# Kernel optimization log

Hardware: AMD Instinct MI355X
Metric: run time of the kernel (lower is better)

## Reference

```python
import jax, jax.numpy as jnp
import numpy as np

N, E, G = 50000, 200000, 2000        # nodes, directed edges, graphs in batch
F_IN, HID, HEADS = 64, 128, 4
DM = HID * HEADS                      # 512, concat GAT output dim
EPS = 1e-5
NEG_SLOPE = 0.2                       # PyG GATConv LeakyReLU slope


def setup_inputs() -> dict:
    key = jax.random.key(0)
    ks = jax.random.split(key, 40)
    rn = lambda k, s, sc: jax.random.normal(k, s, jnp.float32) * sc
    inp = {}
    inp["x"] = rn(ks[0], (N, F_IN), 1.0)
    inp["edge_index"] = jax.random.randint(ks[1], (2, E), 0, N)
    inp["batch"] = jnp.sort(jax.random.randint(ks[2], (N,), 0, G))
    dims = [F_IN, DM, DM]
    for l in range(3):
        d = dims[l]
        inp["W%d" % l] = rn(ks[3 + 4 * l], (d, DM), 1.0 / np.sqrt(d))
        inp["as%d" % l] = rn(ks[4 + 4 * l], (HEADS, HID), 0.1)
        inp["ad%d" % l] = rn(ks[5 + 4 * l], (HEADS, HID), 0.1)
        inp["b%d" % l] = jnp.zeros((DM,), jnp.float32)
        inp["g%d" % l] = jnp.ones((DM,), jnp.float32)
        inp["be%d" % l] = jnp.zeros((DM,), jnp.float32)
    inp["c1w"] = rn(ks[20], (2 * DM, HID), 1.0 / np.sqrt(2 * DM))
    inp["c1b"] = jnp.zeros((HID,), jnp.float32)
    inp["c2w"] = rn(ks[21], (HID, HID // 2), 1.0 / np.sqrt(HID))
    inp["c2b"] = jnp.zeros((HID // 2,), jnp.float32)
    inp["c3w"] = rn(ks[22], (HID // 2, 1), 1.0 / np.sqrt(HID // 2))
    inp["c3b"] = jnp.zeros((1,), jnp.float32)
    return inp


def _gat(x, src, dst, W, a_s, a_d, b):
    """PyG GATConv (heads=HEADS, concat) with self-loops already in src/dst."""
    n = x.shape[0]
    h = (x @ W).reshape(n, HEADS, HID)                     # [N,H,D]
    s_src = jnp.sum(h * a_s, -1)                           # [N,H]
    s_dst = jnp.sum(h * a_d, -1)                           # [N,H]
    e = jax.nn.leaky_relu(s_src[src] + s_dst[dst], NEG_SLOPE)  # [Et,H]
    # segment softmax over incoming edges of each dst node (stable)
    m = jax.lax.stop_gradient(jax.ops.segment_max(e, dst, num_segments=n))
    ex = jnp.exp(e - m[dst])
    alpha = ex / jax.ops.segment_sum(ex, dst, num_segments=n)[dst]
    out = jax.ops.segment_sum(h[src] * alpha[:, :, None], dst, num_segments=n)
    return out.reshape(n, HEADS * HID) + b


def _bn(x, g, b):
    mu = jnp.mean(x, 0)
    var = jnp.var(x, 0)
    return (x - mu) * jax.lax.rsqrt(var + EPS) * g + b


def _forward(x, edge_index, batch, layers, c1w, c1b, c2w, c2b, c3w, c3b):
    loops = jnp.arange(N)
    src = jnp.concatenate([edge_index[0], loops])          # add self-loops
    dst = jnp.concatenate([edge_index[1], loops])
    for (W, a_s, a_d, b, g, be) in layers:
        x = jax.nn.relu(_bn(_gat(x, src, dst, W, a_s, a_d, b), g, be))
    cnt = jax.ops.segment_sum(jnp.ones((N,), x.dtype), batch, num_segments=G)
    mean = jax.ops.segment_sum(x, batch, num_segments=G) / jnp.maximum(cnt, 1.0)[:, None]
    mx = jax.ops.segment_max(x, batch, num_segments=G)
    mx = jnp.where(cnt[:, None] > 0, mx, 0.0)
    h = jnp.concatenate([mean, mx], 1)                     # [G, 2*DM]
    h = jax.nn.relu(h @ c1w + c1b)
    h = jax.nn.relu(h @ c2w + c2b)
    return jax.nn.sigmoid(h @ c3w + c3b).squeeze(-1)       # [G]


def reference(x, edge_index, batch, W0, as0, ad0, b0, g0, be0, W1, as1, ad1, b1, g1, be1, W2, as2, ad2, b2, g2, be2, c1w, c1b, c2w, c2b, c3w, c3b):
    layers = [(W0, as0, ad0, b0, g0, be0), (W1, as1, ad1, b1, g1, be1), (W2, as2, ad2, b2, g2, be2)]
    return _forward(x, edge_index, batch, layers, c1w, c1b, c2w, c2b, c3w, c3b)
```

## Files before the change

### kernel.cpp

```cpp
#include <hip/hip_runtime.h>

#define N_NODES 50000
#define E_EDGES 200000
#define ET_EDGES (E_EDGES + N_NODES)
#define G_GRAPHS 2000
#define F_IN 64
#define HID 128
#define HEADS 4
#define DM 512
#define BN_EPS 1e-5f
#define NEG_SLOPE 0.2f
#define YBLK 391
#define NCHUNK (YBLK / 8)

typedef unsigned short ushort_t;
typedef float floatx4 __attribute__((ext_vector_type(4)));
typedef short short8 __attribute__((ext_vector_type(8)));

__device__ __forceinline__ float b2f(unsigned int u) {
    union { unsigned int i; float f; } v; v.i = u << 16; return v.f;
}
__device__ __forceinline__ ushort_t f2b(float f) {
    union { float f; unsigned int i; } v; v.f = f;
    unsigned int r = v.i + 0x7FFFu + ((v.i >> 16) & 1u);
    return (ushort_t)(r >> 16);
}
__device__ __forceinline__ void unpack8(uint4 v, float* f) {
    f[0] = b2f(v.x & 0xffffu); f[1] = b2f(v.x >> 16);
    f[2] = b2f(v.y & 0xffffu); f[3] = b2f(v.y >> 16);
    f[4] = b2f(v.z & 0xffffu); f[5] = b2f(v.z >> 16);
    f[6] = b2f(v.w & 0xffffu); f[7] = b2f(v.w >> 16);
}
__device__ __forceinline__ void glds16(const ushort_t* g, ushort_t* l) {
    __builtin_amdgcn_global_load_lds(
        (const __attribute__((address_space(1))) unsigned int*)g,
        (__attribute__((address_space(3))) unsigned int*)l, 16, 0, 0);
}

#define XN (N_NODES * F_IN)
#define W0N (F_IN * DM)
#define W1N (DM * DM)
__global__ __launch_bounds__(256) void k_prep(const float* __restrict__ x,
                                              const float* __restrict__ w0,
                                              const float* __restrict__ w1,
                                              const float* __restrict__ w2,
                                              ushort_t* __restrict__ Xb,
                                              ushort_t* __restrict__ Wh0,
                                              ushort_t* __restrict__ Wh1,
                                              ushort_t* __restrict__ Wh2) {
    int t = blockIdx.x * 256 + threadIdx.x;
    if (t < XN) { Xb[t] = f2b(x[t]); return; }
    t -= XN;
    if (t < W0N) {
        int k = t >> 9, n = t & 511;
        Wh0[(size_t)n * F_IN + k] = f2b(w0[t]);
        return;
    }
    t -= W0N;
    if (t < W1N) {
        int k = t >> 9, n = t & 511;
        Wh1[(size_t)n * DM + k] = f2b(w1[t]);
        return;
    }
    t -= W1N;
    if (t < W1N) {
        int k = t >> 9, n = t & 511;
        Wh2[(size_t)n * DM + k] = f2b(w2[t]);
    }
}

__global__ __launch_bounds__(256) void k_wsprep(const float* __restrict__ w0,
                                                const float* __restrict__ as0, const float* __restrict__ ad0,
                                                const float* __restrict__ w1,
                                                const float* __restrict__ as1, const float* __restrict__ ad1,
                                                const float* __restrict__ w2,
                                                const float* __restrict__ as2, const float* __restrict__ ad2,
                                                ushort_t* __restrict__ ws0,
                                                ushort_t* __restrict__ ws1,
                                                ushort_t* __restrict__ ws2) {
    int b = blockIdx.x;
    int l = b >> 3, h = (b >> 1) & 3, v = b & 1;
    const float* w = l == 0 ? w0 : l == 1 ? w1 : w2;
    const float* a = v == 0 ? (l == 0 ? as0 : l == 1 ? as1 : as2)
                            : (l == 0 ? ad0 : l == 1 ? ad1 : ad2);
    ushort_t* o = l == 0 ? ws0 : l == 1 ? ws1 : ws2;
    int K = l == 0 ? F_IN : DM;
    __shared__ float av[HID];
    int t = threadIdx.x;
    if (t < HID) av[t] = a[h * HID + t];
    __syncthreads();
    for (int k = t; k < K; k += 256) {
        const float* wr = w + (size_t)k * DM + h * HID;
        float s = 0.f;
#pragma unroll 8
        for (int c = 0; c < HID; ++c) s += wr[c] * av[c];
        o[(h * 2 + v) * K + k] = f2b(s);
    }
}

__global__ __launch_bounds__(256) void k_mgemm(const ushort_t* __restrict__ A,
                                               const ushort_t* __restrict__ Bh,
                                               const ushort_t* __restrict__ ws,
                                               ushort_t* __restrict__ C,
                                               float* __restrict__ ssrc,
                                               float* __restrict__ sdst,
                                               int M, int K) {
    __shared__ __align__(16) ushort_t Ash[3][128 * 32];
    __shared__ __align__(16) ushort_t Bsh[3][128 * 32];
    __shared__ __align__(16) ushort_t wsh[2 * 512];
    int bid = blockIdx.x;
    int head, yb;
    if (bid < NCHUNK * 32) {
        int chunk = bid >> 5, pos = bid & 31;
        yb = chunk * 8 + (pos & 7);
        head = pos >> 3;
    } else {
        int rem = bid - NCHUNK * 32;
        head = rem & 3;
        yb = NCHUNK * 8 + (rem >> 2);
    }
    int m0 = yb * 128, n0 = head * 128;
    int tid = threadIdx.x;
    int lane = tid & 63, wave = tid >> 6;
    int wm = (wave >> 1) * 64, wn = (wave & 1) * 64;
    floatx4 acc[4][4] = {};
    floatx4 sacc[4] = {};
    for (int i = tid; i < 2 * K; i += 256)
        wsh[i] = ws[(size_t)head * 2 * K + i];
    int lrow = lane >> 2, lchunk = lane & 3;
    int fs = (lrow & 3) ^ ((lrow >> 2) & 3);
    int schunk = lchunk ^ fs;
    int ar0 = wave * 16 + lrow;
    int ar1 = ar0 + 64;
    int gr0 = m0 + ar0; if (gr0 >= M) gr0 = M - 1;
    int gr1 = m0 + ar1; if (gr1 >= M) gr1 = M - 1;
    const ushort_t* gA0 = A + (size_t)gr0 * K + schunk * 8;
    const ushort_t* gA1 = A + (size_t)gr1 * K + schunk * 8;
    const ushort_t* gB0 = Bh + (size_t)(n0 + ar0) * K + schunk * 8;
    const ushort_t* gB1 = Bh + (size_t)(n0 + ar1) * K + schunk * 8;
    int rF = lane & 15, q = lane >> 4;
    int swz = ((q ^ (rF & 3) ^ ((rF >> 2) & 3))) * 8;
    ushort_t* As0 = &Ash[0][0]; ushort_t* As1 = &Ash[1][0]; ushort_t* As2 = &Ash[2][0];
    ushort_t* Bs0 = &Bsh[0][0]; ushort_t* Bs1 = &Bsh[1][0]; ushort_t* Bs2 = &Bsh[2][0];
    auto STAGE = [&](ushort_t* Ab, ushort_t* Bb, int koff) {
        glds16(gA0 + koff, Ab + (wave * 16) * 32);
        glds16(gA1 + koff, Ab + (wave * 16 + 64) * 32);
        glds16(gB0 + koff, Bb + (wave * 16) * 32);
        glds16(gB1 + koff, Bb + (wave * 16 + 64) * 32);
    };
    __syncthreads();
    STAGE(As0, Bs0, 0);
    if (K > 32) STAGE(As1, Bs1, 32);
    for (int k0 = 0; k0 < K; k0 += 32) {
        if (k0 + 32 < K) asm volatile("s_waitcnt vmcnt(4)" ::: "memory");
        else             asm volatile("s_waitcnt vmcnt(0)" ::: "memory");
        __builtin_amdgcn_s_barrier();
        __builtin_amdgcn_sched_barrier(0);
        if (k0 + 64 < K) STAGE(As2, Bs2, k0 + 64);
        short8 sf = *(const short8*)&wsh[(rF & 1) * K + q * 8 + k0];
        short8 af[4], bf[4];
#pragma unroll
        for (int i = 0; i < 4; ++i)
            af[i] = *(const short8*)&As0[(wm + i * 16 + rF) * 32 + swz];
#pragma unroll
        for (int j = 0; j < 4; ++j)
            bf[j] = *(const short8*)&Bs0[(wn + j * 16 + rF) * 32 + swz];
#pragma unroll
        for (int i = 0; i < 4; ++i) {
            sacc[i] = __builtin_amdgcn_mfma_f32_16x16x32_bf16(af[i], sf, sacc[i], 0, 0, 0);
#pragma unroll
            for (int j = 0; j < 4; ++j)
                acc[i][j] = __builtin_amdgcn_mfma_f32_16x16x32_bf16(af[i], bf[j], acc[i][j], 0, 0, 0);
        }
        ushort_t* tA = As0; As0 = As1; As1 = As2; As2 = tA;
        ushort_t* tB = Bs0; Bs0 = Bs1; Bs1 = Bs2; Bs2 = tB;
    }
    int cr = (lane >> 4) * 4, cc = lane & 15;
#pragma unroll
    for (int i = 0; i < 4; ++i) {
#pragma unroll
        for (int r = 0; r < 4; ++r) {
            int gr = m0 + wm + i * 16 + cr + r;
            if (gr < M) {
#pragma unroll
                for (int j = 0; j < 4; ++j)
                    C[(size_t)gr * DM + n0 + wn + j * 16 + cc] = f2b(acc[i][j][r]);
                if (cc == 0) ssrc[gr * 4 + head] = sacc[i][r];
                else if (cc == 1) sdst[gr * 4 + head] = sacc[i][r];
            }
        }
    }
}

__global__ __launch_bounds__(256) void k_bnapply(const ushort_t* __restrict__ X,
                                                 const float* __restrict__ stat,
                                                 const float* __restrict__ gam,
                                                 const float* __restrict__ bet,
                                                 ushort_t* __restrict__ Y) {
    __shared__ float sc[512], sh[512];
    int t = threadIdx.x;
    for (int f = t; f < 512; f += 256) {
        float mu = stat[f] * (1.f / (float)N_NODES);
        float var = fmaxf(stat[512 + f] * (1.f / (float)N_NODES) - mu * mu, 0.f);
        float rs = rsqrtf(var + BN_EPS);
        float s = gam[f] * rs;
        sc[f] = s;
        sh[f] = bet[f] - mu * s;
    }
    __syncthreads();
    int c8 = (t & 63) * 8;
    const float* scp = sc + c8;
    const float* shp = sh + c8;
    for (int n = blockIdx.x * 4 + (t >> 6); n < N_NODES; n += gridDim.x * 4) {
        uint4 v = *(const uint4*)&X[(size_t)n * DM + c8];
        float fv[8]; unpack8(v, fv);
        uint4 ov; unsigned* po = (unsigned*)&ov;
#pragma unroll
        for (int j = 0; j < 4; ++j) {
            unsigned lo = f2b(fmaxf(fv[2 * j] * scp[2 * j] + shp[2 * j], 0.f));
            unsigned hi = f2b(fmaxf(fv[2 * j + 1] * scp[2 * j + 1] + shp[2 * j + 1], 0.f));
            po[j] = lo | (hi << 16);
        }
        *(uint4*)&Y[(size_t)n * DM + c8] = ov;
    }
}

__global__ void k_degree(const int* __restrict__ ei, int* __restrict__ deg) {
    int e = blockIdx.x * blockDim.x + threadIdx.x;
    if (e >= ET_EDGES) return;
    int d = (e < E_EDGES) ? ei[E_EDGES + e] : (e - E_EDGES);
    atomicAdd(&deg[d], 1);
}

__global__ __launch_bounds__(1024) void k_scan3(const int* __restrict__ deg,
                                                int* __restrict__ offs,
                                                int* __restrict__ cursor) {
    __shared__ int wsum[16];
    __shared__ int carry;
    int t = threadIdx.x;
    int lane = t & 63, wv = t >> 6;
    if (t == 0) carry = 0;
    __syncthreads();
    for (int base = 0; base < N_NODES; base += 1024) {
        int i = base + t;
        int v = (i < N_NODES) ? deg[i] : 0;
        int x = v;
#pragma unroll
        for (int off = 1; off < 64; off <<= 1) {
            int y = __shfl_up(x, off);
            if (lane >= off) x += y;
        }
        if (lane == 63) wsum[wv] = x;
        __syncthreads();
        int wpre = 0;
#pragma unroll
        for (int w = 0; w < 16; ++w) wpre += (w < wv) ? wsum[w] : 0;
        int incl = wpre + x;
        if (i < N_NODES) { int o = carry + (incl - v); offs[i] = o; cursor[i] = o; }
        __syncthreads();
        if (t == 1023) carry += incl;
        __syncthreads();
    }
    if (t == 0) offs[N_NODES] = carry;
}

__global__ void k_scatter(const int* __restrict__ ei, int* __restrict__ cursor,
                          int* __restrict__ csr_src) {
    int e = blockIdx.x * blockDim.x + threadIdx.x;
    if (e >= ET_EDGES) return;
    int sv, d;
    if (e < E_EDGES) { sv = ei[e]; d = ei[E_EDGES + e]; } else { sv = d = e - E_EDGES; }
    int pos = atomicAdd(&cursor[d], 1);
    csr_src[pos] = sv;
}

__global__ void k_gbounds(const int* __restrict__ batch, int* __restrict__ gstart) {
    int i = blockIdx.x * blockDim.x + threadIdx.x;
    if (i >= N_NODES) return;
    int b = batch[i];
    int p = (i == 0) ? -1 : batch[i - 1];
    for (int g = p + 1; g <= b; ++g) gstart[g] = i;
    if (i == N_NODES - 1)
        for (int g = b + 1; g <= G_GRAPHS; ++g) gstart[g] = N_NODES;
}

__global__ __launch_bounds__(256) void k_aggregate(const ushort_t* __restrict__ H,
                                                   const float* __restrict__ ssrc,
                                                   const float* __restrict__ sdst,
                                                   const int* __restrict__ offs,
                                                   const int* __restrict__ csr_src,
                                                   const float* __restrict__ bias,
                                                   ushort_t* __restrict__ out) {
    int wave = threadIdx.x >> 6, lane = threadIdx.x & 63;
    int n = blockIdx.x * 4 + wave;
    if (n >= N_NODES) return;
    int beg = offs[n], end = offs[n + 1];
    int hl = lane >> 4, li = lane & 15;
    float sdh = sdst[n * 4 + hl];
    float m = -1e30f, s = 0.f;
    for (int e = beg + li; e < end; e += 16) {
        float sc = ssrc[csr_src[e] * 4 + hl] + sdh;
        sc = sc > 0.f ? sc : NEG_SLOPE * sc;
        if (sc > m) { s = s * __expf(m - sc) + 1.f; m = sc; }
        else s += __expf(sc - m);
    }
#pragma unroll
    for (int mk = 1; mk < 16; mk <<= 1) {
        float om = __shfl_xor(m, mk), os = __shfl_xor(s, mk);
        float mn = fmaxf(m, om);
        s = s * __expf(m - mn) + os * __expf(om - mn);
        m = mn;
    }
    float mh = m, inv = 1.f / s;
    float acc[8] = { 0.f, 0.f, 0.f, 0.f, 0.f, 0.f, 0.f, 0.f };
    int e = beg;
    for (; e + 4 <= end; e += 4) {
        int sv0 = csr_src[e], sv1 = csr_src[e + 1];
        int sv2 = csr_src[e + 2], sv3 = csr_src[e + 3];
        float s0 = ssrc[sv0 * 4 + hl], s1 = ssrc[sv1 * 4 + hl];
        float s2 = ssrc[sv2 * 4 + hl], s3 = ssrc[sv3 * 4 + hl];
        uint4 h0 = *(const uint4*)&H[(size_t)sv0 * DM + lane * 8];
        uint4 h1 = *(const uint4*)&H[(size_t)sv1 * DM + lane * 8];
        uint4 h2 = *(const uint4*)&H[(size_t)sv2 * DM + lane * 8];
        uint4 h3 = *(const uint4*)&H[(size_t)sv3 * DM + lane * 8];
        s0 += sdh; s0 = s0 > 0.f ? s0 : NEG_SLOPE * s0;
        s1 += sdh; s1 = s1 > 0.f ? s1 : NEG_SLOPE * s1;
        s2 += sdh; s2 = s2 > 0.f ? s2 : NEG_SLOPE * s2;
        s3 += sdh; s3 = s3 > 0.f ? s3 : NEG_SLOPE * s3;
        float a0 = __expf(s0 - mh) * inv, a1 = __expf(s1 - mh) * inv;
        float a2 = __expf(s2 - mh) * inv, a3 = __expf(s3 - mh) * inv;
        float f0[8], f1[8], f2[8], f3[8];
        unpack8(h0, f0); unpack8(h1, f1); unpack8(h2, f2); unpack8(h3, f3);
#pragma unroll
        for (int j = 0; j < 8; ++j)
            acc[j] += a0 * f0[j] + a1 * f1[j] + a2 * f2[j] + a3 * f3[j];
    }
    for (; e < end; ++e) {
        int sv = csr_src[e];
        float sc = ssrc[sv * 4 + hl] + sdh;
        sc = sc > 0.f ? sc : NEG_SLOPE * sc;
        float alpha = __expf(sc - mh) * inv;
        uint4 hv = *(const uint4*)&H[(size_t)sv * DM + lane * 8];
        float f[8]; unpack8(hv, f);
#pragma unroll
        for (int j = 0; j < 8; ++j) acc[j] += alpha * f[j];
    }
    const float* bp = bias + lane * 8;
    float4 b0 = *(const float4*)bp;
    float4 b1 = *(const float4*)(bp + 4);
    acc[0] += b0.x; acc[1] += b0.y; acc[2] += b0.z; acc[3] += b0.w;
    acc[4] += b1.x; acc[5] += b1.y; acc[6] += b1.z; acc[7] += b1.w;
    uint4 ov; unsigned* po = (unsigned*)&ov;
#pragma unroll
    for (int j = 0; j < 4; ++j)
        po[j] = (unsigned)f2b(acc[2 * j]) | ((unsigned)f2b(acc[2 * j + 1]) << 16);
    *(uint4*)&out[(size_t)n * DM + lane * 8] = ov;
}

#define BN_ROWS 125
__global__ __launch_bounds__(256) void k_bnstats(const ushort_t* __restrict__ X,
                                                 float* __restrict__ stat) {
    int t = threadIdx.x;
    int c2 = t * 2;
    int beg = blockIdx.x * BN_ROWS;
    int end = beg + BN_ROWS; if (end > N_NODES) end = N_NODES;
    float s0 = 0.f, s1 = 0.f, q0 = 0.f, q1 = 0.f;
    for (int n = beg; n < end; ++n) {
        unsigned v = *(const unsigned*)&X[(size_t)n * DM + c2];
        float x0 = b2f(v & 0xffffu), x1 = b2f(v >> 16);
        s0 += x0; s1 += x1;
        q0 += x0 * x0; q1 += x1 * x1;
    }
    atomicAdd(&stat[c2], s0);
    atomicAdd(&stat[c2 + 1], s1);
    atomicAdd(&stat[512 + c2], q0);
    atomicAdd(&stat[512 + c2 + 1], q1);
}

__global__ __launch_bounds__(64) void k_pool(const ushort_t* __restrict__ X,
                                             const int* __restrict__ gstart,
                                             const float* __restrict__ stat,
                                             const float* __restrict__ gam,
                                             const float* __restrict__ bet,
                                             float* __restrict__ pool) {
    int g = blockIdx.x, t = threadIdx.x;
    int beg = gstart[g], end = gstart[g + 1];
    float sc[8], sh[8];
#pragma unroll
    for (int j = 0; j < 8; ++j) {
        int f = t * 8 + j;
        float mu = stat[f] * (1.f / (float)N_NODES);
        float var = fmaxf(stat[512 + f] * (1.f / (float)N_NODES) - mu * mu, 0.f);
        float rs = rsqrtf(var + BN_EPS);
        sc[j] = gam[f] * rs;
        sh[j] = bet[f] - mu * sc[j];
    }
    float sum[8] = { 0 }, mx[8];
#pragma unroll
    for (int j = 0; j < 8; ++j) mx[j] = -1e30f;
    for (int nn = beg; nn < end; ++nn) {
        uint4 xv = *(const uint4*)&X[(size_t)nn * DM + t * 8];
        float f[8]; unpack8(xv, f);
#pragma unroll
        for (int j = 0; j < 8; ++j) {
            f[j] = fmaxf(f[j] * sc[j] + sh[j], 0.f);
            sum[j] += f[j]; mx[j] = fmaxf(mx[j], f[j]);
        }
    }
    float cnt = (float)(end - beg);
    float inv = cnt > 0.f ? 1.f / cnt : 0.f;
#pragma unroll
    for (int j = 0; j < 8; ++j) {
        pool[(size_t)g * 1024 + t * 8 + j] = sum[j] * inv;
        pool[(size_t)g * 1024 + 512 + t * 8 + j] = cnt > 0.f ? mx[j] : 0.f;
    }
}

__global__ __launch_bounds__(256) void k_mlp(const float* __restrict__ pool,
                                             const float* __restrict__ c1w,
                                             const float* __restrict__ c1b,
                                             const float* __restrict__ c2w,
                                             const float* __restrict__ c2b,
                                             const float* __restrict__ c3w,
                                             const float* __restrict__ c3b,
                                             float* __restrict__ out) {
    __shared__ float row[1024];
    __shared__ float part[128];
    __shared__ float h1[128];
    __shared__ float h2[64];
    int g = blockIdx.x, t = threadIdx.x;
    for (int i = t; i < 1024; i += 256) row[i] = pool[(size_t)g * 1024 + i];
    __syncthreads();
    int half = t >> 7, c = t & 127;
    int k0 = half * 512;
    float a1 = 0.f;
#pragma unroll 8
    for (int k = 0; k < 512; ++k) a1 += row[k0 + k] * c1w[(k0 + k) * 128 + c];
    if (half) part[c] = a1;
    __syncthreads();
    if (!half) h1[c] = fmaxf(a1 + part[c] + c1b[c], 0.f);
    __syncthreads();
    if (t < 64) {
        float a2 = c2b[t];
#pragma unroll 8
        for (int k = 0; k < 128; ++k) a2 += h1[k] * c2w[k * 64 + t];
        h2[t] = fmaxf(a2, 0.f);
    }
    __syncthreads();
    if (t < 64) {
        float p = h2[t] * c3w[t];
#pragma unroll
        for (int off = 32; off > 0; off >>= 1) p += __shfl_down(p, off);
        if (t == 0) {
            float z = p + c3b[0];
            out[g] = 1.f / (1.f + __expf(-z));
        }
    }
}

extern "C" void kernel_launch(void* const* d_in, const int* in_sizes, int n_in,
                              void* d_out, int out_size, void* d_ws, size_t ws_size,
                              hipStream_t stream) {
    const float* x = (const float*)d_in[0];
    const int* ei = (const int*)d_in[1];
    const int* batch = (const int*)d_in[2];
    const float* c1w = (const float*)d_in[21];
    const float* c1b = (const float*)d_in[22];
    const float* c2w = (const float*)d_in[23];
    const float* c2b = (const float*)d_in[24];
    const float* c3w = (const float*)d_in[25];
    const float* c3b = (const float*)d_in[26];

    char* p = (char*)d_ws;
    auto carve = [&](size_t bytes) -> char* {
        char* r = p; p += (bytes + 255) & ~(size_t)255; return r;
    };
    ushort_t* buf0   = (ushort_t*)carve((size_t)N_NODES * DM * 2);
    ushort_t* buf1   = (ushort_t*)carve((size_t)N_NODES * DM * 2);
    ushort_t* Xb     = (ushort_t*)carve((size_t)N_NODES * F_IN * 2);
    ushort_t* Wh0    = (ushort_t*)carve((size_t)F_IN * DM * 2);
    ushort_t* Wh1    = (ushort_t*)carve((size_t)DM * DM * 2);
    ushort_t* Wh2    = (ushort_t*)carve((size_t)DM * DM * 2);
    ushort_t* ws0    = (ushort_t*)carve((size_t)8 * F_IN * 2);
    ushort_t* ws1    = (ushort_t*)carve((size_t)8 * DM * 2);
    ushort_t* ws2    = (ushort_t*)carve((size_t)8 * DM * 2);
    float*    ssrc   = (float*)carve((size_t)N_NODES * 4 * 4);
    float*    sdst   = (float*)carve((size_t)N_NODES * 4 * 4);
    int*      deg    = (int*)carve((size_t)N_NODES * 4);
    int*      offs   = (int*)carve((size_t)(N_NODES + 1) * 4);
    int*      cursor = (int*)carve((size_t)N_NODES * 4);
    int*      csrsrc = (int*)carve((size_t)ET_EDGES * 4);
    float*    bnstat = (float*)carve(3 * 1024 * 4);
    int*      gstart = (int*)carve((size_t)(G_GRAPHS + 1) * 4);
    float*    pool   = (float*)carve((size_t)G_GRAPHS * 1024 * 4);

    hipMemsetAsync(deg, 0, (size_t)N_NODES * 4, stream);
    hipMemsetAsync(bnstat, 0, 3 * 1024 * 4, stream);
    k_degree<<<(ET_EDGES + 255) / 256, 256, 0, stream>>>(ei, deg);
    k_scan3<<<1, 1024, 0, stream>>>(deg, offs, cursor);
    k_scatter<<<(ET_EDGES + 255) / 256, 256, 0, stream>>>(ei, cursor, csrsrc);
    k_gbounds<<<(N_NODES + 255) / 256, 256, 0, stream>>>(batch, gstart);
    {
        int total = XN + W0N + 2 * W1N;
        k_prep<<<(total + 255) / 256, 256, 0, stream>>>(
            x, (const float*)d_in[3], (const float*)d_in[9], (const float*)d_in[15],
            Xb, Wh0, Wh1, Wh2);
    }
    k_wsprep<<<24, 256, 0, stream>>>(
        (const float*)d_in[3], (const float*)d_in[4], (const float*)d_in[5],
        (const float*)d_in[9], (const float*)d_in[10], (const float*)d_in[11],
        (const float*)d_in[15], (const float*)d_in[16], (const float*)d_in[17],
        ws0, ws1, ws2);

    const ushort_t* Whs[3] = { Wh0, Wh1, Wh2 };
    const ushort_t* wss[3] = { ws0, ws1, ws2 };
    const float* pgam = nullptr;
    const float* pbet = nullptr;
    const ushort_t* in = Xb;
    for (int l = 0; l < 3; ++l) {
        int K = (l == 0) ? F_IN : DM;
        const float* bia = (const float*)d_in[6 + 6 * l];
        const float* gam = (const float*)d_in[7 + 6 * l];
        const float* bet = (const float*)d_in[8 + 6 * l];
        ushort_t* h   = (l % 2 == 0) ? buf1 : buf0;
        ushort_t* agg = (l % 2 == 0) ? buf0 : buf1;

        k_mgemm<<<4 * YBLK, 256, 0, stream>>>(
            in, Whs[l], wss[l], h, ssrc, sdst, N_NODES, K);
        k_aggregate<<<(N_NODES + 3) / 4, 256, 0, stream>>>(h, ssrc, sdst, offs, csrsrc, bia, agg);
        k_bnstats<<<(N_NODES + BN_ROWS - 1) / BN_ROWS, 256, 0, stream>>>(agg, bnstat + l * 1024);
        if (l < 2)
            k_bnapply<<<2048, 256, 0, stream>>>(agg, bnstat + l * 1024, gam, bet, h);
        in = h;
        pgam = gam; pbet = bet;
    }
    k_pool<<<G_GRAPHS, 64, 0, stream>>>(buf0, gstart, bnstat + 2 * 1024, pgam, pbet, pool);
    k_mlp<<<G_GRAPHS, 256, 0, stream>>>(pool, c1w, c1b, c2w, c2b, c3w, c3b,
                                        (float*)d_out);
}
```

Baseline: 707.9 us.

## Fuse BN stats into aggregation, parallelize CSR scan, fuse pooling with MLP

Three changes. The single-block serial prefix scan becomes a three-kernel multi-block scan. BatchNorm sum and sum-of-squares are accumulated inside the aggregation kernel, with each wave handling 8 nodes and per-block atomics, so the separate stats pass that re-read the 50000x512 activation is gone. Graph pooling is merged into the MLP kernel so the intermediate pool buffer and one launch disappear. The costs are fewer blocks in aggregation (32 nodes per block) and statistics taken from fp32 accumulators before bf16 rounding, which differs slightly from the old path.

```diff
diff --git a/kernel.cpp b/kernel.cpp
--- a/kernel.cpp
+++ b/kernel.cpp
@@ -12,6 +12,8 @@
 #define NEG_SLOPE 0.2f
 #define YBLK 391
 #define NCHUNK (YBLK / 8)
+#define NBLK 49
+#define AGG_NPB 32
 
 typedef unsigned short ushort_t;
 typedef float floatx4 __attribute__((ext_vector_type(4)));
@@ -232,36 +234,63 @@
     atomicAdd(&deg[d], 1);
 }
 
-__global__ __launch_bounds__(1024) void k_scan3(const int* __restrict__ deg,
+__global__ __launch_bounds__(1024) void k_scanA(const int* __restrict__ deg,
+                                                int* __restrict__ bsum) {
+    __shared__ int wsum[16];
+    int t = threadIdx.x, lane = t & 63, wv = t >> 6;
+    int i = blockIdx.x * 1024 + t;
+    int v = (i < N_NODES) ? deg[i] : 0;
+#pragma unroll
+    for (int off = 32; off > 0; off >>= 1) v += __shfl_down(v, off);
+    if (lane == 0) wsum[wv] = v;
+    __syncthreads();
+    if (t == 0) {
+        int s = 0;
+#pragma unroll
+        for (int w = 0; w < 16; ++w) s += wsum[w];
+        bsum[blockIdx.x] = s;
+    }
+}
+
+__global__ __launch_bounds__(64) void k_scanB(const int* __restrict__ bsum,
+                                              int* __restrict__ bpre,
+                                              int* __restrict__ offs) {
+    int l = threadIdx.x;
+    int v = (l < NBLK) ? bsum[l] : 0;
+    int x = v;
+#pragma unroll
+    for (int off = 1; off < 64; off <<= 1) {
+        int y = __shfl_up(x, off);
+        if (l >= off) x += y;
+    }
+    if (l < NBLK) bpre[l] = x - v;
+    if (l == NBLK - 1) offs[N_NODES] = x;
+}
+
+__global__ __launch_bounds__(1024) void k_scanC(const int* __restrict__ deg,
+                                                const int* __restrict__ bpre,
                                                 int* __restrict__ offs,
                                                 int* __restrict__ cursor) {
     __shared__ int wsum[16];
-    __shared__ int carry;
-    int t = threadIdx.x;
-    int lane = t & 63, wv = t >> 6;
-    if (t == 0) carry = 0;
-    __syncthreads();
-    for (int base = 0; base < N_NODES; base += 1024) {
-        int i = base + t;
-        int v = (i < N_NODES) ? deg[i] : 0;
-        int x = v;
-#pragma unroll
-        for (int off = 1; off < 64; off <<= 1) {
-            int y = __shfl_up(x, off);
-            if (lane >= off) x += y;
-        }
-        if (lane == 63) wsum[wv] = x;
-        __syncthreads();
-        int wpre = 0;
-#pragma unroll
-        for (int w = 0; w < 16; ++w) wpre += (w < wv) ? wsum[w] : 0;
-        int incl = wpre + x;
-        if (i < N_NODES) { int o = carry + (incl - v); offs[i] = o; cursor[i] = o; }
-        __syncthreads();
-        if (t == 1023) carry += incl;
-        __syncthreads();
-    }
-    if (t == 0) offs[N_NODES] = carry;
+    int t = threadIdx.x, lane = t & 63, wv = t >> 6;
+    int i = blockIdx.x * 1024 + t;
+    int v = (i < N_NODES) ? deg[i] : 0;
+    int x = v;
+#pragma unroll
+    for (int off = 1; off < 64; off <<= 1) {
+        int y = __shfl_up(x, off);
+        if (lane >= off) x += y;
+    }
+    if (lane == 63) wsum[wv] = x;
+    __syncthreads();
+    int wpre = 0;
+#pragma unroll
+    for (int w = 0; w < 16; ++w) wpre += (w < wv) ? wsum[w] : 0;
+    int incl = wpre + x;
+    if (i < N_NODES) {
+        int o = bpre[blockIdx.x] + incl - v;
+        offs[i] = o; cursor[i] = o;
+    }
 }
 
 __global__ void k_scatter(const int* __restrict__ ei, int* __restrict__ cursor,
@@ -284,152 +313,142 @@
         for (int g = b + 1; g <= G_GRAPHS; ++g) gstart[g] = N_NODES;
 }
 
-__global__ __launch_bounds__(256) void k_aggregate(const ushort_t* __restrict__ H,
-                                                   const float* __restrict__ ssrc,
-                                                   const float* __restrict__ sdst,
-                                                   const int* __restrict__ offs,
-                                                   const int* __restrict__ csr_src,
-                                                   const float* __restrict__ bias,
-                                                   ushort_t* __restrict__ out) {
-    int wave = threadIdx.x >> 6, lane = threadIdx.x & 63;
-    int n = blockIdx.x * 4 + wave;
-    if (n >= N_NODES) return;
-    int beg = offs[n], end = offs[n + 1];
+__global__ __launch_bounds__(256) void k_aggstats(const ushort_t* __restrict__ H,
+                                                  const float* __restrict__ ssrc,
+                                                  const float* __restrict__ sdst,
+                                                  const int* __restrict__ offs,
+                                                  const int* __restrict__ csr_src,
+                                                  const float* __restrict__ bias,
+                                                  ushort_t* __restrict__ out,
+                                                  float* __restrict__ stat) {
+    __shared__ float sS[4][512], sQ[4][512];
+    int tid = threadIdx.x;
+    int wave = tid >> 6, lane = tid & 63;
     int hl = lane >> 4, li = lane & 15;
-    float sdh = sdst[n * 4 + hl];
-    float m = -1e30f, s = 0.f;
-    for (int e = beg + li; e < end; e += 16) {
-        float sc = ssrc[csr_src[e] * 4 + hl] + sdh;
-        sc = sc > 0.f ? sc : NEG_SLOPE * sc;
-        if (sc > m) { s = s * __expf(m - sc) + 1.f; m = sc; }
-        else s += __expf(sc - m);
-    }
-#pragma unroll
-    for (int mk = 1; mk < 16; mk <<= 1) {
-        float om = __shfl_xor(m, mk), os = __shfl_xor(s, mk);
-        float mn = fmaxf(m, om);
-        s = s * __expf(m - mn) + os * __expf(om - mn);
-        m = mn;
-    }
-    float mh = m, inv = 1.f / s;
-    float acc[8] = { 0.f, 0.f, 0.f, 0.f, 0.f, 0.f, 0.f, 0.f };
-    int e = beg;
-    for (; e + 4 <= end; e += 4) {
-        int sv0 = csr_src[e], sv1 = csr_src[e + 1];
-        int sv2 = csr_src[e + 2], sv3 = csr_src[e + 3];
-        float s0 = ssrc[sv0 * 4 + hl], s1 = ssrc[sv1 * 4 + hl];
-        float s2 = ssrc[sv2 * 4 + hl], s3 = ssrc[sv3 * 4 + hl];
-        uint4 h0 = *(const uint4*)&H[(size_t)sv0 * DM + lane * 8];
-        uint4 h1 = *(const uint4*)&H[(size_t)sv1 * DM + lane * 8];
-        uint4 h2 = *(const uint4*)&H[(size_t)sv2 * DM + lane * 8];
-        uint4 h3 = *(const uint4*)&H[(size_t)sv3 * DM + lane * 8];
-        s0 += sdh; s0 = s0 > 0.f ? s0 : NEG_SLOPE * s0;
-        s1 += sdh; s1 = s1 > 0.f ? s1 : NEG_SLOPE * s1;
-        s2 += sdh; s2 = s2 > 0.f ? s2 : NEG_SLOPE * s2;
-        s3 += sdh; s3 = s3 > 0.f ? s3 : NEG_SLOPE * s3;
-        float a0 = __expf(s0 - mh) * inv, a1 = __expf(s1 - mh) * inv;
-        float a2 = __expf(s2 - mh) * inv, a3 = __expf(s3 - mh) * inv;
-        float f0[8], f1[8], f2[8], f3[8];
-        unpack8(h0, f0); unpack8(h1, f1); unpack8(h2, f2); unpack8(h3, f3);
-#pragma unroll
-        for (int j = 0; j < 8; ++j)
-            acc[j] += a0 * f0[j] + a1 * f1[j] + a2 * f2[j] + a3 * f3[j];
-    }
-    for (; e < end; ++e) {
-        int sv = csr_src[e];
-        float sc = ssrc[sv * 4 + hl] + sdh;
-        sc = sc > 0.f ? sc : NEG_SLOPE * sc;
-        float alpha = __expf(sc - mh) * inv;
-        uint4 hv = *(const uint4*)&H[(size_t)sv * DM + lane * 8];
-        float f[8]; unpack8(hv, f);
-#pragma unroll
-        for (int j = 0; j < 8; ++j) acc[j] += alpha * f[j];
-    }
     const float* bp = bias + lane * 8;
     float4 b0 = *(const float4*)bp;
     float4 b1 = *(const float4*)(bp + 4);
-    acc[0] += b0.x; acc[1] += b0.y; acc[2] += b0.z; acc[3] += b0.w;
-    acc[4] += b1.x; acc[5] += b1.y; acc[6] += b1.z; acc[7] += b1.w;
-    uint4 ov; unsigned* po = (unsigned*)&ov;
-#pragma unroll
-    for (int j = 0; j < 4; ++j)
-        po[j] = (unsigned)f2b(acc[2 * j]) | ((unsigned)f2b(acc[2 * j + 1]) << 16);
-    *(uint4*)&out[(size_t)n * DM + lane * 8] = ov;
-}
-
-#define BN_ROWS 125
-__global__ __launch_bounds__(256) void k_bnstats(const ushort_t* __restrict__ X,
-                                                 float* __restrict__ stat) {
-    int t = threadIdx.x;
-    int c2 = t * 2;
-    int beg = blockIdx.x * BN_ROWS;
-    int end = beg + BN_ROWS; if (end > N_NODES) end = N_NODES;
-    float s0 = 0.f, s1 = 0.f, q0 = 0.f, q1 = 0.f;
-    for (int n = beg; n < end; ++n) {
-        unsigned v = *(const unsigned*)&X[(size_t)n * DM + c2];
-        float x0 = b2f(v & 0xffffu), x1 = b2f(v >> 16);
-        s0 += x0; s1 += x1;
-        q0 += x0 * x0; q1 += x1 * x1;
-    }
-    atomicAdd(&stat[c2], s0);
-    atomicAdd(&stat[c2 + 1], s1);
-    atomicAdd(&stat[512 + c2], q0);
-    atomicAdd(&stat[512 + c2 + 1], q1);
-}
-
-__global__ __launch_bounds__(64) void k_pool(const ushort_t* __restrict__ X,
-                                             const int* __restrict__ gstart,
-                                             const float* __restrict__ stat,
-                                             const float* __restrict__ gam,
-                                             const float* __restrict__ bet,
-                                             float* __restrict__ pool) {
-    int g = blockIdx.x, t = threadIdx.x;
-    int beg = gstart[g], end = gstart[g + 1];
-    float sc[8], sh[8];
+    float sa[8] = { 0.f }, qa[8] = { 0.f };
+    int nbase = blockIdx.x * AGG_NPB + wave * 8;
+    for (int ni = 0; ni < 8; ++ni) {
+        int n = nbase + ni;
+        if (n < N_NODES) {
+            int beg = offs[n], end = offs[n + 1];
+            float sdh = sdst[n * 4 + hl];
+            float m = -1e30f, s = 0.f;
+            for (int e = beg + li; e < end; e += 16) {
+                float sc = ssrc[csr_src[e] * 4 + hl] + sdh;
+                sc = sc > 0.f ? sc : NEG_SLOPE * sc;
+                if (sc > m) { s = s * __expf(m - sc) + 1.f; m = sc; }
+                else s += __expf(sc - m);
+            }
+#pragma unroll
+            for (int mk = 1; mk < 16; mk <<= 1) {
+                float om = __shfl_xor(m, mk), os = __shfl_xor(s, mk);
+                float mn = fmaxf(m, om);
+                s = s * __expf(m - mn) + os * __expf(om - mn);
+                m = mn;
+            }
+            float mh = m, inv = 1.f / s;
+            float acc[8] = { 0.f, 0.f, 0.f, 0.f, 0.f, 0.f, 0.f, 0.f };
+            int e = beg;
+            for (; e + 4 <= end; e += 4) {
+                int sv0 = csr_src[e], sv1 = csr_src[e + 1];
+                int sv2 = csr_src[e + 2], sv3 = csr_src[e + 3];
+                float s0 = ssrc[sv0 * 4 + hl], s1 = ssrc[sv1 * 4 + hl];
+                float s2 = ssrc[sv2 * 4 + hl], s3 = ssrc[sv3 * 4 + hl];
+                uint4 h0 = *(const uint4*)&H[(size_t)sv0 * DM + lane * 8];
+                uint4 h1 = *(const uint4*)&H[(size_t)sv1 * DM + lane * 8];
+                uint4 h2 = *(const uint4*)&H[(size_t)sv2 * DM + lane * 8];
+                uint4 h3 = *(const uint4*)&H[(size_t)sv3 * DM + lane * 8];
+                s0 += sdh; s0 = s0 > 0.f ? s0 : NEG_SLOPE * s0;
+                s1 += sdh; s1 = s1 > 0.f ? s1 : NEG_SLOPE * s1;
+                s2 += sdh; s2 = s2 > 0.f ? s2 : NEG_SLOPE * s2;
+                s3 += sdh; s3 = s3 > 0.f ? s3 : NEG_SLOPE * s3;
+                float a0 = __expf(s0 - mh) * inv, a1 = __expf(s1 - mh) * inv;
+                float a2 = __expf(s2 - mh) * inv, a3 = __expf(s3 - mh) * inv;
+                float f0[8], f1[8], f2[8], f3[8];
+                unpack8(h0, f0); unpack8(h1, f1); unpack8(h2, f2); unpack8(h3, f3);
+#pragma unroll
+                for (int j = 0; j < 8; ++j)
+                    acc[j] += a0 * f0[j] + a1 * f1[j] + a2 * f2[j] + a3 * f3[j];
+            }
+            for (; e < end; ++e) {
+                int sv = csr_src[e];
+                float sc = ssrc[sv * 4 + hl] + sdh;
+                sc = sc > 0.f ? sc : NEG_SLOPE * sc;
+                float alpha = __expf(sc - mh) * inv;
+                uint4 hv = *(const uint4*)&H[(size_t)sv * DM + lane * 8];
+                float f[8]; unpack8(hv, f);
+#pragma unroll
+                for (int j = 0; j < 8; ++j) acc[j] += alpha * f[j];
+            }
+            acc[0] += b0.x; acc[1] += b0.y; acc[2] += b0.z; acc[3] += b0.w;
+            acc[4] += b1.x; acc[5] += b1.y; acc[6] += b1.z; acc[7] += b1.w;
+            uint4 ov; unsigned* po = (unsigned*)&ov;
+#pragma unroll
+            for (int j = 0; j < 4; ++j)
+                po[j] = (unsigned)f2b(acc[2 * j]) | ((unsigned)f2b(acc[2 * j + 1]) << 16);
+            *(uint4*)&out[(size_t)n * DM + lane * 8] = ov;
+#pragma unroll
+            for (int j = 0; j < 8; ++j) {
+                sa[j] += acc[j];
+                qa[j] += acc[j] * acc[j];
+            }
+        }
+    }
 #pragma unroll
     for (int j = 0; j < 8; ++j) {
-        int f = t * 8 + j;
-        float mu = stat[f] * (1.f / (float)N_NODES);
-        float var = fmaxf(stat[512 + f] * (1.f / (float)N_NODES) - mu * mu, 0.f);
-        float rs = rsqrtf(var + BN_EPS);
-        sc[j] = gam[f] * rs;
-        sh[j] = bet[f] - mu * sc[j];
-    }
-    float sum[8] = { 0 }, mx[8];
-#pragma unroll
-    for (int j = 0; j < 8; ++j) mx[j] = -1e30f;
-    for (int nn = beg; nn < end; ++nn) {
-        uint4 xv = *(const uint4*)&X[(size_t)nn * DM + t * 8];
-        float f[8]; unpack8(xv, f);
-#pragma unroll
-        for (int j = 0; j < 8; ++j) {
-            f[j] = fmaxf(f[j] * sc[j] + sh[j], 0.f);
-            sum[j] += f[j]; mx[j] = fmaxf(mx[j], f[j]);
-        }
-    }
-    float cnt = (float)(end - beg);
-    float inv = cnt > 0.f ? 1.f / cnt : 0.f;
-#pragma unroll
-    for (int j = 0; j < 8; ++j) {
-        pool[(size_t)g * 1024 + t * 8 + j] = sum[j] * inv;
-        pool[(size_t)g * 1024 + 512 + t * 8 + j] = cnt > 0.f ? mx[j] : 0.f;
-    }
-}
-
-__global__ __launch_bounds__(256) void k_mlp(const float* __restrict__ pool,
-                                             const float* __restrict__ c1w,
-                                             const float* __restrict__ c1b,
-                                             const float* __restrict__ c2w,
-                                             const float* __restrict__ c2b,
-                                             const float* __restrict__ c3w,
-                                             const float* __restrict__ c3b,
-                                             float* __restrict__ out) {
+        sS[wave][lane * 8 + j] = sa[j];
+        sQ[wave][lane * 8 + j] = qa[j];
+    }
+    __syncthreads();
+    for (int f = tid; f < 512; f += 256) {
+        atomicAdd(&stat[f], sS[0][f] + sS[1][f] + sS[2][f] + sS[3][f]);
+        atomicAdd(&stat[512 + f], sQ[0][f] + sQ[1][f] + sQ[2][f] + sQ[3][f]);
+    }
+}
+
+__global__ __launch_bounds__(256) void k_poolmlp(const ushort_t* __restrict__ X,
+                                                 const int* __restrict__ gstart,
+                                                 const float* __restrict__ stat,
+                                                 const float* __restrict__ gam,
+                                                 const float* __restrict__ bet,
+                                                 const float* __restrict__ c1w,
+                                                 const float* __restrict__ c1b,
+                                                 const float* __restrict__ c2w,
+                                                 const float* __restrict__ c2b,
+                                                 const float* __restrict__ c3w,
+                                                 const float* __restrict__ c3b,
+                                                 float* __restrict__ out) {
     __shared__ float row[1024];
     __shared__ float part[128];
     __shared__ float h1[128];
     __shared__ float h2[64];
     int g = blockIdx.x, t = threadIdx.x;
-    for (int i = t; i < 1024; i += 256) row[i] = pool[(size_t)g * 1024 + i];
+    int beg = gstart[g], end = gstart[g + 1];
+    int f0 = t * 2;
+    float mu0 = stat[f0] * (1.f / (float)N_NODES);
+    float va0 = fmaxf(stat[512 + f0] * (1.f / (float)N_NODES) - mu0 * mu0, 0.f);
+    float sc0 = gam[f0] * rsqrtf(va0 + BN_EPS);
+    float sh0 = bet[f0] - mu0 * sc0;
+    float mu1 = stat[f0 + 1] * (1.f / (float)N_NODES);
+    float va1 = fmaxf(stat[512 + f0 + 1] * (1.f / (float)N_NODES) - mu1 * mu1, 0.f);
+    float sc1 = gam[f0 + 1] * rsqrtf(va1 + BN_EPS);
+    float sh1 = bet[f0 + 1] - mu1 * sc1;
+    float s0 = 0.f, s1 = 0.f, m0 = -1e30f, m1 = -1e30f;
+    for (int nn = beg; nn < end; ++nn) {
+        unsigned v = *(const unsigned*)&X[(size_t)nn * DM + f0];
+        float x0 = fmaxf(b2f(v & 0xffffu) * sc0 + sh0, 0.f);
+        float x1 = fmaxf(b2f(v >> 16) * sc1 + sh1, 0.f);
+        s0 += x0; s1 += x1;
+        m0 = fmaxf(m0, x0); m1 = fmaxf(m1, x1);
+    }
+    float cnt = (float)(end - beg);
+    float inv = cnt > 0.f ? 1.f / cnt : 0.f;
+    row[f0] = s0 * inv;             row[f0 + 1] = s1 * inv;
+    row[512 + f0] = cnt > 0.f ? m0 : 0.f;
+    row[512 + f0 + 1] = cnt > 0.f ? m1 : 0.f;
     __syncthreads();
     int half = t >> 7, c = t & 127;
     int k0 = half * 512;
@@ -492,12 +511,15 @@
     int*      csrsrc = (int*)carve((size_t)ET_EDGES * 4);
     float*    bnstat = (float*)carve(3 * 1024 * 4);
     int*      gstart = (int*)carve((size_t)(G_GRAPHS + 1) * 4);
-    float*    pool   = (float*)carve((size_t)G_GRAPHS * 1024 * 4);
+    int*      bsum   = (int*)carve(64 * 4);
+    int*      bpre   = (int*)carve(64 * 4);
 
     hipMemsetAsync(deg, 0, (size_t)N_NODES * 4, stream);
     hipMemsetAsync(bnstat, 0, 3 * 1024 * 4, stream);
     k_degree<<<(ET_EDGES + 255) / 256, 256, 0, stream>>>(ei, deg);
-    k_scan3<<<1, 1024, 0, stream>>>(deg, offs, cursor);
+    k_scanA<<<NBLK, 1024, 0, stream>>>(deg, bsum);
+    k_scanB<<<1, 64, 0, stream>>>(bsum, bpre, offs);
+    k_scanC<<<NBLK, 1024, 0, stream>>>(deg, bpre, offs, cursor);
     k_scatter<<<(ET_EDGES + 255) / 256, 256, 0, stream>>>(ei, cursor, csrsrc);
     k_gbounds<<<(N_NODES + 255) / 256, 256, 0, stream>>>(batch, gstart);
     {
@@ -527,14 +549,15 @@
 
         k_mgemm<<<4 * YBLK, 256, 0, stream>>>(
             in, Whs[l], wss[l], h, ssrc, sdst, N_NODES, K);
-        k_aggregate<<<(N_NODES + 3) / 4, 256, 0, stream>>>(h, ssrc, sdst, offs, csrsrc, bia, agg);
-        k_bnstats<<<(N_NODES + BN_ROWS - 1) / BN_ROWS, 256, 0, stream>>>(agg, bnstat + l * 1024);
+        k_aggstats<<<(N_NODES + AGG_NPB - 1) / AGG_NPB, 256, 0, stream>>>(
+            h, ssrc, sdst, offs, csrsrc, bia, agg, bnstat + l * 1024);
         if (l < 2)
             k_bnapply<<<2048, 256, 0, stream>>>(agg, bnstat + l * 1024, gam, bet, h);
         in = h;
         pgam = gam; pbet = bet;
     }
-    k_pool<<<G_GRAPHS, 64, 0, stream>>>(buf0, gstart, bnstat + 2 * 1024, pgam, pbet, pool);
-    k_mlp<<<G_GRAPHS, 256, 0, stream>>>(pool, c1w, c1b, c2w, c2b, c3w, c3b,
-                                        (float*)d_out);
-}
+    k_poolmlp<<<G_GRAPHS, 256, 0, stream>>>(buf0, gstart, bnstat + 2 * 1024,
+                                            pgam, pbet,
+                                            c1w, c1b, c2w, c2b, c3w, c3b,
+                                            (float*)d_out);
+}
```

Result: faster. 617.3 us (-12.8%).
